# Performance work log

Hardware: AMD Instinct MI355X
Metric: run time of the kernel (lower is better)

The kernel has to match this reference:

```python
import jax, jax.numpy as jnp
import numpy as np

DIM = 1024
HEADS = 8
DIM_HEAD = 64
INNER = HEADS * DIM_HEAD  # 512


def setup_inputs() -> dict:
    key = jax.random.key(0)
    k1, k2, k3, k4 = jax.random.split(key, 4)
    x = jax.random.normal(k1, (4, 4096, DIM), dtype=jnp.float32)
    W_qkv = jax.random.normal(k2, (DIM, 3 * INNER), dtype=jnp.float32) * (DIM ** -0.5)
    W_out = jax.random.normal(k3, (INNER, DIM), dtype=jnp.float32) * (INNER ** -0.5)
    b_out = jax.random.normal(k4, (DIM,), dtype=jnp.float32) * 0.01
    return {"x": x, "W_qkv": W_qkv, "W_out": W_out, "b_out": b_out}


def reference(x, W_qkv, W_out, b_out):
    b, n, _ = x.shape
    qkv = x @ W_qkv                                   # [b, n, 3*inner]
    q, k, v = jnp.split(qkv, 3, axis=-1)              # each [b, n, inner]

    def to_heads(t):
        return t.reshape(b, n, HEADS, DIM_HEAD).transpose(0, 2, 1, 3)  # [b, h, n, d]

    q = jax.nn.elu(to_heads(q)) + 1.0
    k = jax.nn.elu(to_heads(k)) + 1.0
    v = to_heads(v)
    # kv summary matrix: [b, h, d, e]
    context = jnp.einsum('bhnd,bhne->bhde', k, v)
    out = jnp.einsum('bhde,bhnd->bhne', context, q)   # [b, h, n, e]
    out = out.transpose(0, 2, 1, 3).reshape(b, n, INNER)
    return out @ W_out + b_out
```

## Files before the change

kernel.cpp:

```cpp
#include <hip/hip_runtime.h>
#include <hip/hip_bf16.h>
#include <cstdint>

typedef __attribute__((ext_vector_type(4))) float f32x4;
typedef __attribute__((ext_vector_type(8))) short bf16x8;

__device__ __forceinline__ ushort f2bf(float f) {
  unsigned u = __builtin_bit_cast(unsigned, f);
  u += 0x7fffu + ((u >> 16) & 1u);
  return (ushort)(u >> 16);
}
__device__ __forceinline__ float bf2f(ushort h) {
  unsigned u = ((unsigned)h) << 16;
  return __builtin_bit_cast(float, u);
}

__device__ __forceinline__ void gload_lds16(const ushort* g, ushort* l) {
  __builtin_amdgcn_global_load_lds(
      (const __attribute__((address_space(1))) unsigned int*)g,
      (__attribute__((address_space(3))) unsigned int*)l, 16, 0, 0);
}

__device__ __forceinline__ void hard_barrier() {
  __builtin_amdgcn_sched_barrier(0);
  __builtin_amdgcn_s_barrier();
  __builtin_amdgcn_sched_barrier(0);
}

__global__ __launch_bounds__(256) void cvt_x_kernel(const float4* __restrict__ x,
                                                    ushort4* __restrict__ xb, int n4) {
  int stride = gridDim.x * blockDim.x;
  for (int i = blockIdx.x * blockDim.x + threadIdx.x; i < n4; i += stride) {
    float4 f = x[i];
    ushort4 o;
    o.x = f2bf(f.x); o.y = f2bf(f.y); o.z = f2bf(f.z); o.w = f2bf(f.w);
    xb[i] = o;
  }
}

__global__ __launch_bounds__(256) void transpose_w_kernel(const float* __restrict__ W,
                                                          ushort* __restrict__ Wt) {
  __shared__ float tile[32][33];
  int n0 = blockIdx.x * 32;
  int k0 = blockIdx.y * 32;
  int tx = threadIdx.x;
  int ty = threadIdx.y;
  #pragma unroll
  for (int p = 0; p < 4; ++p) {
    int k = k0 + ty + p * 8;
    tile[ty + p * 8][tx] = W[(size_t)k * 1536 + n0 + tx];
  }
  __syncthreads();
  #pragma unroll
  for (int p = 0; p < 4; ++p) {
    int n = n0 + ty + p * 8;
    Wt[(size_t)n * 1024 + k0 + tx] = f2bf(tile[tx][ty + p * 8]);
  }
}

template <int LDA, int LDB, int NT>
__device__ __forceinline__ void gemm_core(const ushort* __restrict__ A,
                                          const ushort* __restrict__ Bt,
                                          int row0, int col0, f32x4 acc[4][4],
                                          ushort* lds) {
  const int tid = threadIdx.x;
  const int l = tid & 63;
  const int wid = tid >> 6;
  const int fr = l & 15;
  const int fq = l >> 4;
  const int wr = wid >> 2;
  const int wc = wid & 3;

  const int scol = ((l & 7) * 8) ^ (((l >> 3) & 7) * 8);
  const ushort* aS = A + (size_t)(row0 + (tid >> 3)) * LDA + scol;
  const ushort* bS = Bt + (size_t)(col0 + (tid >> 3)) * LDB + scol;

  int aRow[4], bRow[4], kx[2];
  #pragma unroll
  for (int m = 0; m < 4; ++m) aRow[m] = (wr * 64 + m * 16 + fr) * 64;
  #pragma unroll
  for (int n = 0; n < 4; ++n) bRow[n] = (wc * 64 + n * 16 + fr) * 64;
  #pragma unroll
  for (int ks = 0; ks < 2; ++ks) kx[ks] = (ks * 32 + fq * 8) ^ ((fr & 7) * 8);

  auto stage = [&](int t) {
    ushort* dst = lds + (t % 3) * 24576 + tid * 8;
    const int ko = t * 64;
    #pragma unroll
    for (int p = 0; p < 2; ++p)
      gload_lds16(aS + (size_t)(p * 64) * LDA + ko, dst + p * 4096);
    #pragma unroll
    for (int p = 0; p < 4; ++p)
      gload_lds16(bS + (size_t)(p * 64) * LDB + ko, dst + 8192 + p * 4096);
  };

  stage(0);
  stage(1);
  asm volatile("s_waitcnt vmcnt(6)" ::: "memory");
  hard_barrier();

  #pragma unroll
  for (int t = 0; t < NT; ++t) {
    if (t + 2 < NT) stage(t + 2);
    const ushort* aB = lds + (t % 3) * 24576;
    const ushort* bB = aB + 8192;
    #pragma unroll
    for (int ks = 0; ks < 2; ++ks) {
      bf16x8 av[4], bv[4];
      #pragma unroll
      for (int m = 0; m < 4; ++m) av[m] = *(const bf16x8*)&aB[aRow[m] + kx[ks]];
      #pragma unroll
      for (int n = 0; n < 4; ++n) bv[n] = *(const bf16x8*)&bB[bRow[n] + kx[ks]];
      __builtin_amdgcn_s_setprio(1);
      #pragma unroll
      for (int m = 0; m < 4; ++m)
        #pragma unroll
        for (int n = 0; n < 4; ++n)
          acc[m][n] = __builtin_amdgcn_mfma_f32_16x16x32_bf16(av[m], bv[n], acc[m][n], 0, 0, 0);
      __builtin_amdgcn_s_setprio(0);
    }
    if (t + 2 < NT) {
      asm volatile("s_waitcnt vmcnt(6)" ::: "memory");
      hard_barrier();
    } else if (t + 1 < NT) {
      asm volatile("s_waitcnt vmcnt(0)" ::: "memory");
      hard_barrier();
    }
  }
}

__global__ __launch_bounds__(512, 2) void gemm_qkv_kernel(const ushort* __restrict__ xb,
                                                          const ushort* __restrict__ wt,
                                                          ushort* __restrict__ qkv) {
  __shared__ ushort lds[73728];
  f32x4 acc[4][4] = {};
  const int row0 = blockIdx.x * 128;
  const int col0 = blockIdx.y * 256;
  gemm_core<1024, 1024, 16>(xb, wt, row0, col0, acc, lds);
  const int l = threadIdx.x & 63;
  const int wid = threadIdx.x >> 6;
  const int wr = wid >> 2, wc = wid & 3;
  const int fr = l & 15, fq = l >> 4;
  #pragma unroll
  for (int m = 0; m < 4; ++m) {
    #pragma unroll
    for (int n = 0; n < 4; ++n) {
      const int c = col0 + wc * 64 + n * 16 + fr;
      #pragma unroll
      for (int j = 0; j < 4; ++j) {
        const int r = row0 + wr * 64 + m * 16 + fq * 4 + j;
        float v = acc[m][n][j];
        if (c < 1024) v = (v > 0.f) ? (v + 1.f) : __expf(v);
        qkv[(size_t)r * 1536 + c] = f2bf(v);
      }
    }
  }
}

__global__ __launch_bounds__(256) void ctx_kernel(const ushort* __restrict__ qkv,
                                                  float* __restrict__ part) {
  const int bh = blockIdx.x;
  const int split = blockIdx.y;
  const int b = bh >> 3, h = bh & 7;
  const int t = threadIdx.x;
  const int d0 = (t >> 4) * 4;
  const int e0 = (t & 15) * 4;
  __shared__ ushort ks[64][64];
  __shared__ ushort vs[64][64];
  float acc[4][4] = {};
  const int rowBase = b * 4096 + split * 256;
  for (int chunk = 0; chunk < 256; chunk += 64) {
    __syncthreads();
    #pragma unroll
    for (int p = 0; p < 2; ++p) {
      const int r = (t >> 3) + p * 32;
      const int c = (t & 7) * 8;
      const ushort* src = qkv + (size_t)(rowBase + chunk + r) * 1536;
      *(uint4*)&ks[r][c] = *(const uint4*)(src + 512 + h * 64 + c);
      *(uint4*)&vs[r][c] = *(const uint4*)(src + 1024 + h * 64 + c);
    }
    __syncthreads();
    for (int r = 0; r < 64; ++r) {
      ushort4 ku = *(const ushort4*)&ks[r][d0];
      ushort4 vu = *(const ushort4*)&vs[r][e0];
      float kk[4] = {bf2f(ku.x), bf2f(ku.y), bf2f(ku.z), bf2f(ku.w)};
      float vv[4] = {bf2f(vu.x), bf2f(vu.y), bf2f(vu.z), bf2f(vu.w)};
      #pragma unroll
      for (int i = 0; i < 4; ++i)
        #pragma unroll
        for (int j = 0; j < 4; ++j)
          acc[i][j] += kk[i] * vv[j];
    }
  }
  float* dst = part + ((size_t)split * 32 + bh) * 4096;
  #pragma unroll
  for (int i = 0; i < 4; ++i)
    #pragma unroll
    for (int j = 0; j < 4; ++j)
      dst[(d0 + i) * 64 + (e0 + j)] = acc[i][j];
}

__global__ __launch_bounds__(256) void ctx_reduce_kernel(const float* __restrict__ part,
                                                         float* __restrict__ ctx) {
  const int i = blockIdx.x * 256 + threadIdx.x;
  float s = 0.f;
  #pragma unroll
  for (int sp = 0; sp < 16; ++sp) s += part[(size_t)sp * 131072 + i];
  ctx[i] = s;
}

__global__ __launch_bounds__(256) void weff_kernel(const float* __restrict__ ctx,
                                                   const float* __restrict__ Wout,
                                                   ushort* __restrict__ weff) {
  const int bh = blockIdx.x;
  const int h = bh & 7;
  const int m0 = blockIdx.y * 128;
  const int t = threadIdx.x;
  __shared__ float cs[64 * 64];
  __shared__ float ws[64][128];
  #pragma unroll
  for (int p = 0; p < 4; ++p) {
    const int idx = p * 1024 + t * 4;
    *(float4*)&cs[idx] = *(const float4*)&ctx[(size_t)bh * 4096 + idx];
  }
  #pragma unroll
  for (int p = 0; p < 8; ++p) {
    const int e = (t >> 5) + p * 8;
    const int c = (t & 31) * 4;
    *(float4*)&ws[e][c] = *(const float4*)&Wout[(size_t)(h * 64 + e) * 1024 + m0 + c];
  }
  __syncthreads();
  const int m = t & 127;
  const int dh = (t >> 7) * 32;
  float acc[32] = {};
  for (int e = 0; e < 64; ++e) {
    const float w = ws[e][m];
    #pragma unroll
    for (int i = 0; i < 32; ++i)
      acc[i] += cs[(dh + i) * 64 + e] * w;
  }
  ushort* dst = weff + ((size_t)(bh >> 3) * 1024 + m0 + m) * 512 + h * 64 + dh;
  #pragma unroll
  for (int i = 0; i < 32; ++i) dst[i] = f2bf(acc[i]);
}

__global__ __launch_bounds__(512, 2) void gemm_out_kernel(const ushort* __restrict__ qkv,
                                                          const ushort* __restrict__ weff,
                                                          const float* __restrict__ bout,
                                                          float* __restrict__ out) {
  __shared__ ushort lds[73728];
  f32x4 acc[4][4] = {};
  const int row0 = blockIdx.x * 128;
  const int col0 = blockIdx.y * 256;
  const int b = row0 >> 12;
  gemm_core<1536, 512, 8>(qkv, weff + (size_t)b * 1024 * 512, row0, col0, acc, lds);
  const int l = threadIdx.x & 63;
  const int wid = threadIdx.x >> 6;
  const int wr = wid >> 2, wc = wid & 3;
  const int fr = l & 15, fq = l >> 4;
  #pragma unroll
  for (int m = 0; m < 4; ++m) {
    #pragma unroll
    for (int n = 0; n < 4; ++n) {
      const int c = col0 + wc * 64 + n * 16 + fr;
      const float bb = bout[c];
      #pragma unroll
      for (int j = 0; j < 4; ++j) {
        const int r = row0 + wr * 64 + m * 16 + fq * 4 + j;
        out[(size_t)r * 1024 + c] = acc[m][n][j] + bb;
      }
    }
  }
}

extern "C" void kernel_launch(void* const* d_in, const int* in_sizes, int n_in,
                              void* d_out, int out_size, void* d_ws, size_t ws_size,
                              hipStream_t stream) {
  const float* x    = (const float*)d_in[0];
  const float* Wqkv = (const float*)d_in[1];
  const float* Wout = (const float*)d_in[2];
  const float* bout = (const float*)d_in[3];
  float* out = (float*)d_out;
  char* ws = (char*)d_ws;

  ushort* xb   = (ushort*)(ws);
  ushort* wt   = (ushort*)(ws + 33554432);
  ushort* qkv  = (ushort*)(ws + 36700160);
  float*  part = (float* )(ws + 87031808);
  float*  ctx  = (float* )(ws + 95420416);
  ushort* weff = (ushort*)(ws + 95944704);

  cvt_x_kernel<<<2048, 256, 0, stream>>>((const float4*)x, (ushort4*)xb, 16384 * 1024 / 4);
  transpose_w_kernel<<<dim3(48, 32), dim3(32, 8), 0, stream>>>(Wqkv, wt);
  gemm_qkv_kernel<<<dim3(128, 6), 512, 0, stream>>>(xb, wt, qkv);
  ctx_kernel<<<dim3(32, 16), 256, 0, stream>>>(qkv, part);
  ctx_reduce_kernel<<<512, 256, 0, stream>>>(part, ctx);
  weff_kernel<<<dim3(32, 8), 256, 0, stream>>>(ctx, Wout, weff);
  gemm_out_kernel<<<dim3(128, 4), 512, 0, stream>>>(qkv, weff, bout, out);
}
```

Baseline: 150.7 us.

## Enlarge GEMM tiles to 256x256 with K=32 stages and a new swizzle

Rewrites the shared GEMM core so each block computes a 256x256 output tile with 8x4 MFMA accumulators per wave, while each pipeline stage shrinks to K=32. LDS use per block drops (3*512*32 halves) and the LDS swizzle and row mapping are redesigned. The grids are halved in the row dimension. The aim is more operand reuse per byte loaded and fewer redundant global loads. The cost is twice the accumulator registers and fewer blocks: 384 and 256, which may underfill 256 CUs at 2 blocks per CU. The tighter vmcnt waits per stage also leave less time to hide load latency.

```diff
diff --git a/kernel.cpp b/kernel.cpp
--- a/kernel.cpp
+++ b/kernel.cpp
@@ -25,6 +25,14 @@
   __builtin_amdgcn_sched_barrier(0);
   __builtin_amdgcn_s_barrier();
   __builtin_amdgcn_sched_barrier(0);
+}
+
+template <int N>
+__device__ __forceinline__ void wait_vm() {
+  if constexpr (N == 0) asm volatile("s_waitcnt vmcnt(0)" ::: "memory");
+  else if constexpr (N == 3) asm volatile("s_waitcnt vmcnt(3)" ::: "memory");
+  else if constexpr (N == 4) asm volatile("s_waitcnt vmcnt(4)" ::: "memory");
+  else static_assert(N < 0, "unsupported vmcnt");
 }
 
 __global__ __launch_bounds__(256) void cvt_x_kernel(const float4* __restrict__ x,
@@ -58,97 +66,109 @@
   }
 }
 
-template <int LDA, int LDB, int NT>
-__device__ __forceinline__ void gemm_core(const ushort* __restrict__ A,
-                                          const ushort* __restrict__ Bt,
-                                          int row0, int col0, f32x4 acc[4][4],
-                                          ushort* lds) {
+template <int MREP, int LDA, int LDB, int NT>
+__device__ __forceinline__ void gemm_core3(const ushort* __restrict__ A,
+                                           const ushort* __restrict__ Bt,
+                                           int row0, int col0, f32x4 acc[MREP][4],
+                                           ushort* lds) {
+  constexpr int BM = MREP * 32;
+  constexpr int SLOT = (BM + 256) * 32;
+  constexpr int ALOADS = BM / 128;
+  constexpr int BLOADS = 2;
+  constexpr int L = ALOADS + BLOADS;
   const int tid = threadIdx.x;
   const int l = tid & 63;
   const int wid = tid >> 6;
-  const int fr = l & 15;
-  const int fq = l >> 4;
-  const int wr = wid >> 2;
-  const int wc = wid & 3;
-
-  const int scol = ((l & 7) * 8) ^ (((l >> 3) & 7) * 8);
-  const ushort* aS = A + (size_t)(row0 + (tid >> 3)) * LDA + scol;
-  const ushort* bS = Bt + (size_t)(col0 + (tid >> 3)) * LDB + scol;
-
-  int aRow[4], bRow[4], kx[2];
-  #pragma unroll
-  for (int m = 0; m < 4; ++m) aRow[m] = (wr * 64 + m * 16 + fr) * 64;
-  #pragma unroll
-  for (int n = 0; n < 4; ++n) bRow[n] = (wc * 64 + n * 16 + fr) * 64;
-  #pragma unroll
-  for (int ks = 0; ks < 2; ++ks) kx[ks] = (ks * 32 + fq * 8) ^ ((fr & 7) * 8);
-
-  auto stage = [&](int t) {
-    ushort* dst = lds + (t % 3) * 24576 + tid * 8;
-    const int ko = t * 64;
-    #pragma unroll
-    for (int p = 0; p < 2; ++p)
-      gload_lds16(aS + (size_t)(p * 64) * LDA + ko, dst + p * 4096);
-    #pragma unroll
-    for (int p = 0; p < 4; ++p)
-      gload_lds16(bS + (size_t)(p * 64) * LDB + ko, dst + 8192 + p * 4096);
+  const int fr = l & 15, fq = l >> 4;
+  const int wr = wid >> 2, wc = wid & 3;
+
+  const int g = tid >> 3;
+  const int slotL = (tid & 7) ^ (g & 7);
+  const int srow = 2 * g + (slotL >> 2);
+  const int scol = (slotL & 3) * 8;
+  const ushort* aSrc[ALOADS];
+  const ushort* bSrc[BLOADS];
+  #pragma unroll
+  for (int p = 0; p < ALOADS; ++p)
+    aSrc[p] = A + (size_t)(row0 + p * 128 + srow) * LDA + scol;
+  #pragma unroll
+  for (int p = 0; p < BLOADS; ++p)
+    bSrc[p] = Bt + (size_t)(col0 + p * 128 + srow) * LDB + scol;
+
+  auto stage = [&](int tt) {
+    ushort* dst = lds + (tt % 3) * SLOT + tid * 8;
+    const int ko = tt * 32;
+    #pragma unroll
+    for (int p = 0; p < ALOADS; ++p) gload_lds16(aSrc[p] + ko, dst + p * 4096);
+    #pragma unroll
+    for (int p = 0; p < BLOADS; ++p) gload_lds16(bSrc[p] + ko, dst + BM * 32 + p * 4096);
+  };
+
+  const int fsl = (((fr & 1) << 2) | fq) ^ (fr >> 1);
+  const int frb = (fr >> 1) * 64 + fsl * 8;
+  const int aOff = wr * (MREP * 512) + frb;
+  const int bOff = BM * 32 + wc * 2048 + frb;
+
+  auto compute = [&](int s) {
+    const ushort* base = lds + s * SLOT;
+    const ushort* aB = base + aOff;
+    const ushort* bB = base + bOff;
+    bf16x8 bv[4];
+    #pragma unroll
+    for (int n = 0; n < 4; ++n) bv[n] = *(const bf16x8*)(bB + n * 512);
+    #pragma unroll
+    for (int mh = 0; mh < MREP / 4; ++mh) {
+      bf16x8 av[4];
+      #pragma unroll
+      for (int mm = 0; mm < 4; ++mm)
+        av[mm] = *(const bf16x8*)(aB + (mh * 4 + mm) * 512);
+      __builtin_amdgcn_s_setprio(1);
+      #pragma unroll
+      for (int mm = 0; mm < 4; ++mm)
+        #pragma unroll
+        for (int n = 0; n < 4; ++n)
+          acc[mh * 4 + mm][n] =
+              __builtin_amdgcn_mfma_f32_16x16x32_bf16(av[mm], bv[n], acc[mh * 4 + mm][n], 0, 0, 0);
+      __builtin_amdgcn_s_setprio(0);
+    }
   };
 
   stage(0);
   stage(1);
-  asm volatile("s_waitcnt vmcnt(6)" ::: "memory");
+  wait_vm<L>();
   hard_barrier();
-
-  #pragma unroll
-  for (int t = 0; t < NT; ++t) {
-    if (t + 2 < NT) stage(t + 2);
-    const ushort* aB = lds + (t % 3) * 24576;
-    const ushort* bB = aB + 8192;
-    #pragma unroll
-    for (int ks = 0; ks < 2; ++ks) {
-      bf16x8 av[4], bv[4];
-      #pragma unroll
-      for (int m = 0; m < 4; ++m) av[m] = *(const bf16x8*)&aB[aRow[m] + kx[ks]];
-      #pragma unroll
-      for (int n = 0; n < 4; ++n) bv[n] = *(const bf16x8*)&bB[bRow[n] + kx[ks]];
-      __builtin_amdgcn_s_setprio(1);
-      #pragma unroll
-      for (int m = 0; m < 4; ++m)
-        #pragma unroll
-        for (int n = 0; n < 4; ++n)
-          acc[m][n] = __builtin_amdgcn_mfma_f32_16x16x32_bf16(av[m], bv[n], acc[m][n], 0, 0, 0);
-      __builtin_amdgcn_s_setprio(0);
-    }
-    if (t + 2 < NT) {
-      asm volatile("s_waitcnt vmcnt(6)" ::: "memory");
-      hard_barrier();
-    } else if (t + 1 < NT) {
-      asm volatile("s_waitcnt vmcnt(0)" ::: "memory");
-      hard_barrier();
-    }
-  }
+  for (int t = 0; t < NT - 2; ++t) {
+    stage(t + 2);
+    compute(t % 3);
+    wait_vm<L>();
+    hard_barrier();
+  }
+  compute((NT - 2) % 3);
+  wait_vm<0>();
+  hard_barrier();
+  compute((NT - 1) % 3);
 }
 
 __global__ __launch_bounds__(512, 2) void gemm_qkv_kernel(const ushort* __restrict__ xb,
                                                           const ushort* __restrict__ wt,
                                                           ushort* __restrict__ qkv) {
-  __shared__ ushort lds[73728];
-  f32x4 acc[4][4] = {};
-  const int row0 = blockIdx.x * 128;
+  __shared__ ushort lds[3 * 512 * 32];
+  f32x4 acc[8][4] = {};
+  const int row0 = blockIdx.x * 256;
   const int col0 = blockIdx.y * 256;
-  gemm_core<1024, 1024, 16>(xb, wt, row0, col0, acc, lds);
+  gemm_core3<8, 1024, 1024, 32>(xb, wt, row0, col0, acc, lds);
   const int l = threadIdx.x & 63;
   const int wid = threadIdx.x >> 6;
   const int wr = wid >> 2, wc = wid & 3;
   const int fr = l & 15, fq = l >> 4;
   #pragma unroll
-  for (int m = 0; m < 4; ++m) {
+  for (int m = 0; m < 8; ++m) {
     #pragma unroll
     for (int n = 0; n < 4; ++n) {
       const int c = col0 + wc * 64 + n * 16 + fr;
       #pragma unroll
       for (int j = 0; j < 4; ++j) {
-        const int r = row0 + wr * 64 + m * 16 + fq * 4 + j;
+        const int r = row0 + wr * 128 + m * 16 + fq * 4 + j;
         float v = acc[m][n][j];
         if (c < 1024) v = (v > 0.f) ? (v + 1.f) : __expf(v);
         qkv[(size_t)r * 1536 + c] = f2bf(v);
@@ -248,25 +268,25 @@
                                                           const ushort* __restrict__ weff,
                                                           const float* __restrict__ bout,
                                                           float* __restrict__ out) {
-  __shared__ ushort lds[73728];
-  f32x4 acc[4][4] = {};
-  const int row0 = blockIdx.x * 128;
+  __shared__ ushort lds[3 * 512 * 32];
+  f32x4 acc[8][4] = {};
+  const int row0 = blockIdx.x * 256;
   const int col0 = blockIdx.y * 256;
   const int b = row0 >> 12;
-  gemm_core<1536, 512, 8>(qkv, weff + (size_t)b * 1024 * 512, row0, col0, acc, lds);
+  gemm_core3<8, 1536, 512, 16>(qkv, weff + (size_t)b * 1024 * 512, row0, col0, acc, lds);
   const int l = threadIdx.x & 63;
   const int wid = threadIdx.x >> 6;
   const int wr = wid >> 2, wc = wid & 3;
   const int fr = l & 15, fq = l >> 4;
   #pragma unroll
-  for (int m = 0; m < 4; ++m) {
+  for (int m = 0; m < 8; ++m) {
     #pragma unroll
     for (int n = 0; n < 4; ++n) {
       const int c = col0 + wc * 64 + n * 16 + fr;
       const float bb = bout[c];
       #pragma unroll
       for (int j = 0; j < 4; ++j) {
-        const int r = row0 + wr * 64 + m * 16 + fq * 4 + j;
+        const int r = row0 + wr * 128 + m * 16 + fq * 4 + j;
         out[(size_t)r * 1024 + c] = acc[m][n][j] + bb;
       }
     }
@@ -292,9 +312,9 @@
 
   cvt_x_kernel<<<2048, 256, 0, stream>>>((const float4*)x, (ushort4*)xb, 16384 * 1024 / 4);
   transpose_w_kernel<<<dim3(48, 32), dim3(32, 8), 0, stream>>>(Wqkv, wt);
-  gemm_qkv_kernel<<<dim3(128, 6), 512, 0, stream>>>(xb, wt, qkv);
+  gemm_qkv_kernel<<<dim3(64, 6), 512, 0, stream>>>(xb, wt, qkv);
   ctx_kernel<<<dim3(32, 16), 256, 0, stream>>>(qkv, part);
   ctx_reduce_kernel<<<512, 256, 0, stream>>>(part, ctx);
   weff_kernel<<<dim3(32, 8), 256, 0, stream>>>(ctx, Wout, weff);
-  gemm_out_kernel<<<dim3(128, 4), 512, 0, stream>>>(qkv, weff, bout, out);
-}
+  gemm_out_kernel<<<dim3(64, 4), 512, 0, stream>>>(qkv, weff, bout, out);
+}
```

Measured after the change: 152.9 us. No clear change (+1.5%).

## Store K and V transposed per head and compute context with MFMA

Applied to the files above, without the earlier changes.

The QKV GEMM epilogue now writes Q as a dense [rows,512] buffer and K/V transposed per batch-head ([bh,64,4096]), so the context reduction over sequence becomes a contiguous-K GEMM. The scalar FMA context kernel is replaced with an MFMA kernel that loads swizzled tiles via global_load_lds across 32 splits. The reduce kernel now sums 32 partials. The partials buffer aliases the x-bf16 buffer. Transposed stores in the epilogue are 8-byte scattered writes, which may cost more in the QKV GEMM than the context kernel saves.

```diff
diff --git a/kernel.cpp b/kernel.cpp
--- a/kernel.cpp
+++ b/kernel.cpp
@@ -10,10 +10,6 @@
   u += 0x7fffu + ((u >> 16) & 1u);
   return (ushort)(u >> 16);
 }
-__device__ __forceinline__ float bf2f(ushort h) {
-  unsigned u = ((unsigned)h) << 16;
-  return __builtin_bit_cast(float, u);
-}
 
 __device__ __forceinline__ void gload_lds16(const ushort* g, ushort* l) {
   __builtin_amdgcn_global_load_lds(
@@ -25,6 +21,19 @@
   __builtin_amdgcn_sched_barrier(0);
   __builtin_amdgcn_s_barrier();
   __builtin_amdgcn_sched_barrier(0);
+}
+
+template <int N>
+__device__ __forceinline__ void wait_vm() {
+  if constexpr (N == 0) asm volatile("s_waitcnt vmcnt(0)" ::: "memory");
+  else if constexpr (N == 2) asm volatile("s_waitcnt vmcnt(2)" ::: "memory");
+  else if constexpr (N == 4) asm volatile("s_waitcnt vmcnt(4)" ::: "memory");
+  else if constexpr (N == 6) asm volatile("s_waitcnt vmcnt(6)" ::: "memory");
+  else static_assert(N < 0, "unsupported vmcnt");
+}
+
+__device__ __forceinline__ float elu1(float v) {
+  return (v > 0.f) ? (v + 1.f) : __expf(v);
 }
 
 __global__ __launch_bounds__(256) void cvt_x_kernel(const float4* __restrict__ x,
@@ -96,7 +105,7 @@
 
   stage(0);
   stage(1);
-  asm volatile("s_waitcnt vmcnt(6)" ::: "memory");
+  wait_vm<6>();
   hard_barrier();
 
   #pragma unroll
@@ -120,10 +129,10 @@
       __builtin_amdgcn_s_setprio(0);
     }
     if (t + 2 < NT) {
-      asm volatile("s_waitcnt vmcnt(6)" ::: "memory");
+      wait_vm<6>();
       hard_barrier();
     } else if (t + 1 < NT) {
-      asm volatile("s_waitcnt vmcnt(0)" ::: "memory");
+      wait_vm<0>();
       hard_barrier();
     }
   }
@@ -131,7 +140,9 @@
 
 __global__ __launch_bounds__(512, 2) void gemm_qkv_kernel(const ushort* __restrict__ xb,
                                                           const ushort* __restrict__ wt,
-                                                          ushort* __restrict__ qkv) {
+                                                          ushort* __restrict__ q,
+                                                          ushort* __restrict__ kT,
+                                                          ushort* __restrict__ vT) {
   __shared__ ushort lds[73728];
   f32x4 acc[4][4] = {};
   const int row0 = blockIdx.x * 128;
@@ -146,58 +157,92 @@
     #pragma unroll
     for (int n = 0; n < 4; ++n) {
       const int c = col0 + wc * 64 + n * 16 + fr;
-      #pragma unroll
-      for (int j = 0; j < 4; ++j) {
-        const int r = row0 + wr * 64 + m * 16 + fq * 4 + j;
-        float v = acc[m][n][j];
-        if (c < 1024) v = (v > 0.f) ? (v + 1.f) : __expf(v);
-        qkv[(size_t)r * 1536 + c] = f2bf(v);
+      const int r0 = row0 + wr * 64 + m * 16 + fq * 4;
+      if (c < 512) {
+        #pragma unroll
+        for (int j = 0; j < 4; ++j)
+          q[(size_t)(r0 + j) * 512 + c] = f2bf(elu1(acc[m][n][j]));
+      } else if (c < 1024) {
+        const int d = c - 512;
+        const int bh = (r0 >> 12) * 8 + (d >> 6);
+        const int nn = r0 & 4095;
+        ushort4 o;
+        o.x = f2bf(elu1(acc[m][n][0]));
+        o.y = f2bf(elu1(acc[m][n][1]));
+        o.z = f2bf(elu1(acc[m][n][2]));
+        o.w = f2bf(elu1(acc[m][n][3]));
+        *(ushort4*)&kT[((size_t)bh * 64 + (d & 63)) * 4096 + nn] = o;
+      } else {
+        const int d = c - 1024;
+        const int bh = (r0 >> 12) * 8 + (d >> 6);
+        const int nn = r0 & 4095;
+        ushort4 o;
+        o.x = f2bf(acc[m][n][0]);
+        o.y = f2bf(acc[m][n][1]);
+        o.z = f2bf(acc[m][n][2]);
+        o.w = f2bf(acc[m][n][3]);
+        *(ushort4*)&vT[((size_t)bh * 64 + (d & 63)) * 4096 + nn] = o;
       }
     }
   }
 }
 
-__global__ __launch_bounds__(256) void ctx_kernel(const ushort* __restrict__ qkv,
-                                                  float* __restrict__ part) {
+__global__ __launch_bounds__(256) void ctx_mfma_kernel(const ushort* __restrict__ kT,
+                                                       const ushort* __restrict__ vT,
+                                                       float* __restrict__ part) {
+  __shared__ ushort lds[16384];
   const int bh = blockIdx.x;
-  const int split = blockIdx.y;
-  const int b = bh >> 3, h = bh & 7;
-  const int t = threadIdx.x;
-  const int d0 = (t >> 4) * 4;
-  const int e0 = (t & 15) * 4;
-  __shared__ ushort ks[64][64];
-  __shared__ ushort vs[64][64];
-  float acc[4][4] = {};
-  const int rowBase = b * 4096 + split * 256;
-  for (int chunk = 0; chunk < 256; chunk += 64) {
-    __syncthreads();
-    #pragma unroll
-    for (int p = 0; p < 2; ++p) {
-      const int r = (t >> 3) + p * 32;
-      const int c = (t & 7) * 8;
-      const ushort* src = qkv + (size_t)(rowBase + chunk + r) * 1536;
-      *(uint4*)&ks[r][c] = *(const uint4*)(src + 512 + h * 64 + c);
-      *(uint4*)&vs[r][c] = *(const uint4*)(src + 1024 + h * 64 + c);
-    }
-    __syncthreads();
-    for (int r = 0; r < 64; ++r) {
-      ushort4 ku = *(const ushort4*)&ks[r][d0];
-      ushort4 vu = *(const ushort4*)&vs[r][e0];
-      float kk[4] = {bf2f(ku.x), bf2f(ku.y), bf2f(ku.z), bf2f(ku.w)};
-      float vv[4] = {bf2f(vu.x), bf2f(vu.y), bf2f(vu.z), bf2f(vu.w)};
-      #pragma unroll
-      for (int i = 0; i < 4; ++i)
-        #pragma unroll
-        for (int j = 0; j < 4; ++j)
-          acc[i][j] += kk[i] * vv[j];
-    }
-  }
-  float* dst = part + ((size_t)split * 32 + bh) * 4096;
-  #pragma unroll
-  for (int i = 0; i < 4; ++i)
-    #pragma unroll
-    for (int j = 0; j < 4; ++j)
-      dst[(d0 + i) * 64 + (e0 + j)] = acc[i][j];
+  const int sp = blockIdx.y;
+  const int tid = threadIdx.x;
+  const int l = tid & 63, wid = tid >> 6;
+  const int fr = l & 15, fq = l >> 4;
+  const int wr = wid >> 1, wc = wid & 1;
+
+  const size_t base = (size_t)bh * 64 * 4096 + sp * 128;
+  const int srow = tid >> 2;
+  const int lam = (tid & 3) ^ ((tid >> 3) & 3);
+  const ushort* aG = kT + base + (size_t)srow * 4096 + lam * 8;
+  const ushort* bG = vT + base + (size_t)srow * 4096 + lam * 8;
+
+  #pragma unroll
+  for (int t = 0; t < 4; ++t) {
+    ushort* d = lds + t * 4096 + tid * 8;
+    gload_lds16(aG + t * 32, d);
+    gload_lds16(bG + t * 32, d + 2048);
+  }
+
+  const int sig = fq ^ ((fr >> 1) & 3);
+  f32x4 acc[2][2] = {};
+
+  auto compute = [&](int t) {
+    const ushort* sb = lds + t * 4096;
+    bf16x8 av[2], bv[2];
+    #pragma unroll
+    for (int mm = 0; mm < 2; ++mm)
+      av[mm] = *(const bf16x8*)&sb[(wr * 32 + mm * 16 + fr) * 32 + sig * 8];
+    #pragma unroll
+    for (int nn = 0; nn < 2; ++nn)
+      bv[nn] = *(const bf16x8*)&sb[2048 + (wc * 32 + nn * 16 + fr) * 32 + sig * 8];
+    #pragma unroll
+    for (int mm = 0; mm < 2; ++mm)
+      #pragma unroll
+      for (int nn = 0; nn < 2; ++nn)
+        acc[mm][nn] = __builtin_amdgcn_mfma_f32_16x16x32_bf16(av[mm], bv[nn], acc[mm][nn], 0, 0, 0);
+  };
+
+  wait_vm<6>(); hard_barrier(); compute(0);
+  wait_vm<4>(); hard_barrier(); compute(1);
+  wait_vm<2>(); hard_barrier(); compute(2);
+  wait_vm<0>(); hard_barrier(); compute(3);
+
+  float* dst = part + ((size_t)sp * 32 + bh) * 4096;
+  #pragma unroll
+  for (int mm = 0; mm < 2; ++mm)
+    #pragma unroll
+    for (int nn = 0; nn < 2; ++nn)
+      #pragma unroll
+      for (int j = 0; j < 4; ++j)
+        dst[(wr * 32 + mm * 16 + fq * 4 + j) * 64 + wc * 32 + nn * 16 + fr] = acc[mm][nn][j];
 }
 
 __global__ __launch_bounds__(256) void ctx_reduce_kernel(const float* __restrict__ part,
@@ -205,7 +250,7 @@
   const int i = blockIdx.x * 256 + threadIdx.x;
   float s = 0.f;
   #pragma unroll
-  for (int sp = 0; sp < 16; ++sp) s += part[(size_t)sp * 131072 + i];
+  for (int sp = 0; sp < 32; ++sp) s += part[(size_t)sp * 131072 + i];
   ctx[i] = s;
 }
 
@@ -244,7 +289,7 @@
   for (int i = 0; i < 32; ++i) dst[i] = f2bf(acc[i]);
 }
 
-__global__ __launch_bounds__(512, 2) void gemm_out_kernel(const ushort* __restrict__ qkv,
+__global__ __launch_bounds__(512, 2) void gemm_out_kernel(const ushort* __restrict__ q,
                                                           const ushort* __restrict__ weff,
                                                           const float* __restrict__ bout,
                                                           float* __restrict__ out) {
@@ -253,7 +298,7 @@
   const int row0 = blockIdx.x * 128;
   const int col0 = blockIdx.y * 256;
   const int b = row0 >> 12;
-  gemm_core<1536, 512, 8>(qkv, weff + (size_t)b * 1024 * 512, row0, col0, acc, lds);
+  gemm_core<512, 512, 8>(q, weff + (size_t)b * 1024 * 512, row0, col0, acc, lds);
   const int l = threadIdx.x & 63;
   const int wid = threadIdx.x >> 6;
   const int wr = wid >> 2, wc = wid & 3;
@@ -284,17 +329,19 @@
   char* ws = (char*)d_ws;
 
   ushort* xb   = (ushort*)(ws);
+  float*  part = (float* )(ws);
   ushort* wt   = (ushort*)(ws + 33554432);
-  ushort* qkv  = (ushort*)(ws + 36700160);
-  float*  part = (float* )(ws + 87031808);
-  float*  ctx  = (float* )(ws + 95420416);
-  ushort* weff = (ushort*)(ws + 95944704);
+  ushort* q    = (ushort*)(ws + 36700160);
+  ushort* kT   = (ushort*)(ws + 53477376);
+  ushort* vT   = (ushort*)(ws + 70254592);
+  float*  ctx  = (float* )(ws + 87031808);
+  ushort* weff = (ushort*)(ws + 87556096);
 
   cvt_x_kernel<<<2048, 256, 0, stream>>>((const float4*)x, (ushort4*)xb, 16384 * 1024 / 4);
   transpose_w_kernel<<<dim3(48, 32), dim3(32, 8), 0, stream>>>(Wqkv, wt);
-  gemm_qkv_kernel<<<dim3(128, 6), 512, 0, stream>>>(xb, wt, qkv);
-  ctx_kernel<<<dim3(32, 16), 256, 0, stream>>>(qkv, part);
+  gemm_qkv_kernel<<<dim3(128, 6), 512, 0, stream>>>(xb, wt, q, kT, vT);
+  ctx_mfma_kernel<<<dim3(32, 32), 256, 0, stream>>>(kT, vT, part);
   ctx_reduce_kernel<<<512, 256, 0, stream>>>(part, ctx);
   weff_kernel<<<dim3(32, 8), 256, 0, stream>>>(ctx, Wout, weff);
-  gemm_out_kernel<<<dim3(128, 4), 512, 0, stream>>>(qkv, weff, bout, out);
-}
+  gemm_out_kernel<<<dim3(128, 4), 512, 0, stream>>>(q, weff, bout, out);
+}
```

New measurement: 136.1 us. -9.7%, faster.
